# Optimization experiments

Hardware: AMD Instinct MI355X
Metric: run time of the kernel (lower is better)

The kernel has to match this reference:

```python
import jax, jax.numpy as jnp
import numpy as np

L = 4096   # num_tokens (one prefill sequence)
D = 2048   # hidden_size
HK = 16    # num_k_heads
HV = 32    # num_v_heads
DK = 128   # head_k_dim
DV = 128   # head_v_dim
RATIO = HV // HK
EPS = 1e-6


def setup_inputs() -> dict:
    key = jax.random.key(0)
    ks = jax.random.split(key, 11)
    s = 0.02
    return {
        "hidden_states": jax.random.normal(ks[0], (L, D), jnp.float32),
        "Wq": jax.random.normal(ks[1], (D, HK * DK), jnp.float32) * s,
        "Wk": jax.random.normal(ks[2], (D, HK * DK), jnp.float32) * s,
        "Wv": jax.random.normal(ks[3], (D, HV * DV), jnp.float32) * s,
        "Wz": jax.random.normal(ks[4], (D, HV * DV), jnp.float32) * s,
        "Wb": jax.random.normal(ks[5], (D, HV), jnp.float32) * s,
        "Wa": jax.random.normal(ks[6], (D, HV), jnp.float32) * s,
        "A_log": jnp.log(jax.random.uniform(ks[7], (HV,), jnp.float32, 1.0, 16.0)),
        "dt_bias": jax.random.normal(ks[8], (HV,), jnp.float32) * 0.5,
        "norm_weight": jnp.ones((DV,), jnp.float32),
        "W_out": jax.random.normal(ks[9], (HV * DV, D), jnp.float32) * s,
    }


def _l2norm(x):
    return x * jax.lax.rsqrt(jnp.sum(x * x, axis=-1, keepdims=True) + EPS)


def reference(hidden_states, Wq, Wk, Wv, Wz, Wb, Wa, A_log, dt_bias, norm_weight, W_out):
    h = hidden_states
    # --- input projections (qkvz + ba split) ---
    q = _l2norm((h @ Wq).reshape(L, HK, DK))            # [L, HK, DK]
    k = _l2norm((h @ Wk).reshape(L, HK, DK))
    v = (h @ Wv).reshape(L, HV, DV)                     # [L, HV, DV]
    z = (h @ Wz).reshape(L, HV, DV)                     # gate for RMSNorm
    beta = jax.nn.sigmoid(h @ Wb)                       # [L, HV]
    g = -jnp.exp(A_log) * jax.nn.softplus(h @ Wa + dt_bias)  # [L, HV]
    decay = jnp.exp(g)                                  # per-token per-head decay
    # repeat shared q/k heads to value heads (GQA ratio)
    q = jnp.repeat(q, RATIO, axis=1) * (DK ** -0.5)     # [L, HV, DK]
    k = jnp.repeat(k, RATIO, axis=1)

    # --- gated delta rule recurrence over tokens ---
    def step(S, xs):
        q_t, k_t, v_t, b_t, d_t = xs                    # [HV,DK],[HV,DK],[HV,DV],[HV],[HV]
        S = S * d_t[:, None, None]                      # decay state [HV, DK, DV]
        pred = jnp.einsum('hk,hkv->hv', k_t, S)         # memory readout
        delta = (v_t - pred) * b_t[:, None]             # delta-rule correction
        S = S + k_t[:, :, None] * delta[:, None, :]
        o = jnp.einsum('hk,hkv->hv', q_t, S)
        return S, o

    S0 = jnp.zeros((HV, DK, DV), jnp.float32)
    _, core = jax.lax.scan(step, S0, (q, k, v, beta, decay))  # core: [L, HV, DV]

    # --- gated RMSNorm: x * silu(z), rms-normalize over head dim ---
    x = core * jax.nn.silu(z)
    x = x * jax.lax.rsqrt(jnp.mean(x * x, axis=-1, keepdims=True) + EPS) * norm_weight

    # --- output projection ---
    return x.reshape(L, HV * DV) @ W_out                # [L, D]
```

## Files before the change

kernel.cpp:

```cpp
#include <hip/hip_runtime.h>

#define LTOK 4096
#define DHID 2048
#define HKN  16
#define HVN  32
#define DKK  128
#define NTOT 12288

typedef unsigned short u16;
typedef __attribute__((ext_vector_type(8))) short short8;
typedef __attribute__((ext_vector_type(8))) unsigned short u16x8;
typedef __attribute__((ext_vector_type(4))) unsigned short u16x4;
typedef __attribute__((ext_vector_type(4))) float f32x4;

__device__ __forceinline__ float b2f(u16 u) {
  unsigned int x = ((unsigned int)u) << 16;
  return __builtin_bit_cast(float, x);
}
__device__ __forceinline__ u16 f2bf(float f) {
  unsigned int u = __builtin_bit_cast(unsigned int, f);
  u += 0x7FFFu + ((u >> 16) & 1u);
  return (u16)(u >> 16);
}

template<int C> __device__ __forceinline__ float dppmv(float x) {
  int i = __builtin_amdgcn_update_dpp(0, __builtin_bit_cast(int, x), C, 0xF, 0xF, true);
  return __builtin_bit_cast(float, i);
}
__device__ __forceinline__ float red16(float x) {
  x += dppmv<0xB1>(x);
  x += dppmv<0x4E>(x);
  x += dppmv<0x124>(x);
  x += dppmv<0x128>(x);
  return x;
}

__device__ __forceinline__ void gld16(const void* g, void* l) {
  __builtin_amdgcn_global_load_lds((const __attribute__((address_space(1))) void*)g,
                                   (__attribute__((address_space(3))) void*)l, 16, 0, 0);
}

template<int OFF> __device__ __forceinline__ short8 dsr(unsigned a) {
  short8 r;
  asm volatile("ds_read_b128 %0, %1 offset:%2" : "=v"(r) : "v"(a), "n"(OFF));
  return r;
}
__device__ __forceinline__ short8 gldx4(const u16* p) {
  short8 r;
  asm volatile("global_load_dwordx4 %0, %1, off" : "=v"(r) : "v"(p));
  return r;
}
#define KEEPV(x) asm volatile("" :: "v"(x))

__device__ __forceinline__ int sw16(int r, int c, int rowc) { return (r * rowc + c) ^ ((r & 7) << 3); }

__device__ __forceinline__ void cstore(u16* C, size_t i, float v) { C[i] = f2bf(v); }
__device__ __forceinline__ void cstore(float* C, size_t i, float v) { C[i] = v; }

__global__ __launch_bounds__(256)
void k_cvt(const float* __restrict__ s, u16* __restrict__ d, int n) {
  const int i = (blockIdx.x * 256 + threadIdx.x) * 4;
  const float4 v = *(const float4*)(s + i);
  ushort4 o;
  o.x = f2bf(v.x); o.y = f2bf(v.y); o.z = f2bf(v.z); o.w = f2bf(v.w);
  *(ushort4*)(d + i) = o;
}

__global__ __launch_bounds__(256)
void k_trf(const float* __restrict__ W, u16* __restrict__ Bf, int Ncols, int nkt, int j16base) {
  const int wv = threadIdx.x >> 6, lane = threadIdx.x & 63;
  const int frag = blockIdx.x * 4 + wv;
  const int j16 = frag / nkt, kt = frag % nkt;
  const int r0 = kt * 32 + (lane >> 4) * 8;
  const int c = j16 * 16 + (lane & 15);
  u16x8 o;
#pragma unroll
  for (int e = 0; e < 8; ++e) o[e] = f2bf(W[(size_t)(r0 + e) * Ncols + c]);
  *(u16x8*)(Bf + ((size_t)(j16base + j16) * nkt + kt) * 512 + lane * 8) = o;
}

#define MFMA16(a, b, c) __builtin_amdgcn_mfma_f32_16x16x32_bf16(a, b, c, 0, 0, 0)

template<typename OutT, int NWM, int NWN>
__global__ __launch_bounds__(NWM * 256, 2)
void k_g256(const u16* __restrict__ A, const u16* __restrict__ Bf, OutT* __restrict__ C,
            int M, int N, int K, int NT) {
  constexpr int BN = NWN * 64;
  constexpr int BUFE = NWM * 4096;
  __shared__ u16 Lds[4 * BUFE];
  const int tid = threadIdx.x;
  const int lane = tid & 63, w = tid >> 6;
  const int fr = lane & 15, fq = lane >> 4;
  const int wm = (w >> 2) * 128, wn = (w & 3) * (NWN * 16);
  const int nkt = K >> 5;
  const size_t sK = (size_t)K;

  const int MT = gridDim.x / NT;
  const int nts = (NT < 16) ? NT : 16;
  const int per_super = MT * nts;
  const int super = blockIdx.x / per_super;
  const int within = blockIdx.x % per_super;
  const int mtg = MT >> 3;
  const int q = within >> 3;
  const int mt = (within & 7) * mtg + (q % mtg);
  const int nt = super * nts + q / mtg;

  const int kslot = ((tid & 3) ^ ((tid >> 3) & 3)) * 8;
  const u16* aS = A + (size_t)(mt * (NWM * 128) + (tid >> 2)) * sK + kslot;

  const int jw = nt * (BN / 16) + (w & 3) * NWN;
  const u16* bp[NWN];
#pragma unroll
  for (int j = 0; j < NWN; ++j) bp[j] = Bf + ((size_t)(jw + j) * nkt) * 512 + lane * 8;

  f32x4 acc[8][NWN] = {};

  auto STAGE = [&](int kt_) {
    const int sk = (kt_ < nkt) ? kt_ : nkt - 1;
    u16* base = &Lds[(kt_ & 3) * BUFE];
    gld16(aS + (size_t)sk * 32, base + tid * 8);
    gld16(aS + (size_t)(NWM * 64) * sK + (size_t)sk * 32, base + NWM * 2048 + tid * 8);
  };

#define LOADB(bset, kt_) {                                                    \
    const int sk2 = ((kt_) < nkt) ? (kt_) : (nkt - 1);                        \
    _Pragma("unroll")                                                         \
    for (int j = 0; j < NWN; ++j) bset[j] = gldx4(bp[j] + (size_t)sk2 * 512); }

  const int akey = (fr >> 1) & 3;
  const unsigned ldsBase = (unsigned)(size_t)(__attribute__((address_space(3))) void*)&Lds[0];
  const unsigned aA0 = ldsBase + 2u * (unsigned)((wm + fr) * 32 + ((fq ^ akey) << 3));

  short8 afA[8], afB[8], bs0[NWN], bs1[NWN];

#define RD(afX, kt_) {                                                        \
    const unsigned aAr = aA0 + (unsigned)(((kt_) & 3) * (BUFE * 2));          \
    afX[0] = dsr<0>(aAr);    afX[1] = dsr<1024>(aAr);                         \
    afX[2] = dsr<2048>(aAr); afX[3] = dsr<3072>(aAr);                         \
    afX[4] = dsr<4096>(aAr); afX[5] = dsr<5120>(aAr);                         \
    afX[6] = dsr<6144>(aAr); afX[7] = dsr<7168>(aAr); }

  STAGE(0); STAGE(1); STAGE(2);
  LOADB(bs0, 0)
  LOADB(bs1, 1)
  asm volatile("s_waitcnt vmcnt(0)" ::: "memory");
  __builtin_amdgcn_s_barrier();
  RD(afA, 0)
  asm volatile("s_waitcnt lgkmcnt(0)" ::: "memory");
  __builtin_amdgcn_sched_barrier(0);

#define ITER(kt_, afC, bC, afN) {                                             \
    STAGE((kt_) + 3);                                                         \
    asm volatile("s_waitcnt vmcnt(%0)" :: "n"(NWN + 4) : "memory");           \
    __builtin_amdgcn_s_barrier();                                             \
    __builtin_amdgcn_sched_barrier(0);                                        \
    RD(afN, (kt_) + 1)                                                        \
    __builtin_amdgcn_sched_barrier(0);                                        \
    __builtin_amdgcn_s_setprio(1);                                            \
    _Pragma("unroll")                                                         \
    for (int i = 0; i < 8; ++i)                                               \
      _Pragma("unroll")                                                       \
      for (int j = 0; j < NWN; ++j)                                           \
        acc[i][j] = MFMA16(afC[i], bC[j], acc[i][j]);                         \
    __builtin_amdgcn_s_setprio(0);                                            \
    LOADB(bC, (kt_) + 2)                                                      \
    asm volatile("s_waitcnt lgkmcnt(0)" ::: "memory");                        \
    __builtin_amdgcn_sched_barrier(0); }

  for (int kt = 0; kt < nkt; kt += 2) {
    ITER(kt, afA, bs0, afB)
    ITER(kt + 1, afB, bs1, afA)
  }
#undef ITER
#undef RD
#undef LOADB

  asm volatile("s_waitcnt vmcnt(0) lgkmcnt(0)" ::: "memory");
  __builtin_amdgcn_sched_barrier(0);
  KEEPV(bs0[0]); KEEPV(bs0[1]);
  if constexpr (NWN == 4) { KEEPV(bs0[2]); KEEPV(bs0[3]); }
  KEEPV(bs1[0]); KEEPV(bs1[1]);
  if constexpr (NWN == 4) { KEEPV(bs1[2]); KEEPV(bs1[3]); }
  KEEPV(afA[0]); KEEPV(afA[1]); KEEPV(afA[2]); KEEPV(afA[3]);
  KEEPV(afA[4]); KEEPV(afA[5]); KEEPV(afA[6]); KEEPV(afA[7]);
  KEEPV(afB[0]); KEEPV(afB[1]); KEEPV(afB[2]); KEEPV(afB[3]);
  KEEPV(afB[4]); KEEPV(afB[5]); KEEPV(afB[6]); KEEPV(afB[7]);

  const int r0 = mt * (NWM * 128) + wm + fq * 4;
  const int c0 = nt * BN + wn + fr;
#pragma unroll
  for (int i = 0; i < 8; ++i)
#pragma unroll
    for (int j = 0; j < NWN; ++j)
#pragma unroll
      for (int e = 0; e < 4; ++e)
        cstore(C, (size_t)(r0 + i * 16 + e) * N + c0 + j * 16, acc[i][j][e]);
}

__global__ __launch_bounds__(256)
void k_ba(const float* __restrict__ h, const float* __restrict__ Wb, const float* __restrict__ Wa,
          const float* __restrict__ A_log, const float* __restrict__ dtb,
          float* __restrict__ beta, float* __restrict__ g_out) {
  const int w = threadIdx.x >> 6, lane = threadIdx.x & 63;
  const int t = blockIdx.x * 4 + w;
  const int j = lane & 31;
  const bool isB = lane < 32;
  const float* __restrict__ hr = h + (size_t)t * DHID;
  const float* Wc = isB ? Wb : Wa;
  float acc = 0.f;
  for (int kk = 0; kk < DHID; ++kk) acc = fmaf(hr[kk], Wc[(size_t)kk * HVN + j], acc);
  if (isB) {
    beta[(size_t)t * HVN + j] = 1.f / (1.f + expf(-acc));
  } else {
    float xx = acc + dtb[j];
    float sp = (xx > 20.f) ? xx : log1pf(expf(xx));
    g_out[(size_t)t * HVN + j] = -expf(A_log[j]) * sp;
  }
}

__global__ __launch_bounds__(256)
void k_l2n(u16* __restrict__ qkvz) {
  const int w = threadIdx.x >> 6, lane = threadIdx.x & 63;
  const int r = blockIdx.x * 4 + w;
  const int isK = r >> 16;
  const int rr = r & 65535;
  const int t = rr >> 4, hd = rr & 15;
  u16* p = qkvz + (size_t)t * NTOT + isK * 2048 + hd * DKK + lane * 2;
  float a = b2f(p[0]), b = b2f(p[1]);
  float ss = a * a + b * b;
  ss = red16(ss);
  ss += __shfl_xor(ss, 16);
  ss += __shfl_xor(ss, 32);
  const float sc = rsqrtf(ss + 1e-6f) * (isK ? 1.f : 0.08838834764831845f);
  p[0] = f2bf(a * sc); p[1] = f2bf(b * sc);
}

__global__ __launch_bounds__(256)
void k_r1(const u16* __restrict__ qkvz, const float* __restrict__ beta_g,
          const float* __restrict__ g_g, u16* __restrict__ UM_g, float* __restrict__ cumL_g) {
  const int pair = blockIdx.x;
  const int hv = pair >> 6, n = pair & 63;
  const int hk = hv >> 1;
  const int t0 = n * 64;
  const int tid = threadIdx.x, lane = tid & 63, wv = tid >> 6;
  const int fr = lane & 15, fq = lane >> 4;

  __shared__ __align__(16) u16 Xb[256 * 64];
  __shared__ __align__(16) u16 Dbuf0[64 * 64 * 2];
  __shared__ __align__(16) u16 Dbuf1[64 * 64 * 2];
  __shared__ float Lc[64];
  __shared__ float Bc[64];
  u16* Kl = Dbuf0;

  const int j = tid & 63, h = tid >> 6;
  const u16* kg = qkvz + (size_t)(t0 + j) * NTOT + 2048 + hk * DKK + h * 32;
  const u16* vg = qkvz + (size_t)(t0 + j) * NTOT + 4096 + hv * DKK + h * 32;
  u16x8 kv[4], vv[4];
#pragma unroll
  for (int i = 0; i < 4; ++i) { kv[i] = *(const u16x8*)(kg + i * 8); vv[i] = *(const u16x8*)(vg + i * 8); }
  if (tid < 64) {
    Lc[tid] = g_g[(size_t)(t0 + tid) * HVN + hv];
    Bc[tid] = beta_g[(size_t)(t0 + tid) * HVN + hv];
  }
#pragma unroll
  for (int i = 0; i < 4; ++i) *(u16x8*)&Kl[sw16(j, h * 32 + i * 8, 128)] = kv[i];
  __syncthreads();
  if (tid == 0) { float a = 0.f; for (int t = 0; t < 64; ++t) { a += Lc[t]; Lc[t] = a; } }
  __syncthreads();
  if (tid < 64) cumL_g[(size_t)pair * 64 + tid] = Lc[tid];

  {
    const float bj = Bc[j];
    const float mj = bj * __expf(Lc[j]);
#pragma unroll
    for (int i = 0; i < 4; ++i)
#pragma unroll
      for (int e = 0; e < 8; ++e) {
        int c = h * 32 + i * 8 + e;
        Xb[sw16(c, j, 64)] = f2bf(bj * b2f(vv[i][e]));
        Xb[sw16(128 + c, j, 64)] = f2bf(mj * b2f(kv[i][e]));
      }
  }
  f32x4 kk[4] = {};
#pragma unroll
  for (int ks = 0; ks < 4; ++ks) {
    short8 afr = *(const short8*)&Kl[sw16(wv * 16 + fr, ks * 32 + fq * 8, 128)];
#pragma unroll
    for (int ct = 0; ct < 4; ++ct) {
      short8 bfr = *(const short8*)&Kl[sw16(ct * 16 + fr, ks * 32 + fq * 8, 128)];
      kk[ct] = MFMA16(afr, bfr, kk[ct]);
    }
  }
  __syncthreads();

  f32x4 acc[16];
#pragma unroll
  for (int ct = 0; ct < 16; ++ct) {
    u16x4 xi = *(const u16x4*)&Xb[sw16(ct * 16 + fr, wv * 16 + fq * 4, 64)];
    acc[ct][0] = b2f(xi[0]); acc[ct][1] = b2f(xi[1]); acc[ct][2] = b2f(xi[2]); acc[ct][3] = b2f(xi[3]);
  }
#pragma unroll
  for (int ct = 0; ct < 4; ++ct) {
    const int s = ct * 16 + fr;
    u16x4 pk;
#pragma unroll
    for (int e = 0; e < 4; ++e) {
      const int t = wv * 16 + fq * 4 + e;
      float v = (s < t) ? -Bc[t] * __expf(Lc[t] - Lc[s]) * kk[ct][e] : 0.f;
      pk[e] = f2bf(v);
      Dbuf0[sw16(t, s, 64)] = pk[e];
    }
    *(u16x4*)&Dbuf0[4096 + sw16(s, wv * 16 + fq * 4, 64)] = pk;
  }
  __syncthreads();

  u16* DA = Dbuf0;
  u16* DB = Dbuf1;
  for (int stg = 0; stg < 6; ++stg) {
    u16* Dr = DA;
    u16* Dc = DA + 4096;
    short8 da0 = *(const short8*)&Dr[sw16(wv * 16 + fr, 0 + fq * 8, 64)];
    short8 da1 = *(const short8*)&Dr[sw16(wv * 16 + fr, 32 + fq * 8, 64)];
#pragma unroll
    for (int ct = 0; ct < 16; ++ct) {
      short8 b0 = *(const short8*)&Xb[sw16(ct * 16 + fr, 0 + fq * 8, 64)];
      short8 b1 = *(const short8*)&Xb[sw16(ct * 16 + fr, 32 + fq * 8, 64)];
      acc[ct] = MFMA16(da0, b0, acc[ct]);
      acc[ct] = MFMA16(da1, b1, acc[ct]);
    }
    f32x4 sq[4] = {};
    if (stg < 5) {
#pragma unroll
      for (int ct = 0; ct < 4; ++ct) {
        short8 sb0 = *(const short8*)&Dc[sw16(ct * 16 + fr, 0 + fq * 8, 64)];
        short8 sb1 = *(const short8*)&Dc[sw16(ct * 16 + fr, 32 + fq * 8, 64)];
        sq[ct] = MFMA16(da0, sb0, sq[ct]);
        sq[ct] = MFMA16(da1, sb1, sq[ct]);
      }
    }
    __syncthreads();
#pragma unroll
    for (int ct = 0; ct < 16; ++ct) {
      u16x4 pk;
      pk[0] = f2bf(acc[ct][0]); pk[1] = f2bf(acc[ct][1]); pk[2] = f2bf(acc[ct][2]); pk[3] = f2bf(acc[ct][3]);
      *(u16x4*)&Xb[sw16(ct * 16 + fr, wv * 16 + fq * 4, 64)] = pk;
    }
    if (stg < 5) {
#pragma unroll
      for (int ct = 0; ct < 4; ++ct) {
        u16x4 pk;
        pk[0] = f2bf(sq[ct][0]); pk[1] = f2bf(sq[ct][1]); pk[2] = f2bf(sq[ct][2]); pk[3] = f2bf(sq[ct][3]);
        *(u16x4*)&(DB + 4096)[sw16(ct * 16 + fr, wv * 16 + fq * 4, 64)] = pk;
#pragma unroll
        for (int e = 0; e < 4; ++e) DB[sw16(wv * 16 + fq * 4 + e, ct * 16 + fr, 64)] = pk[e];
      }
    }
    __syncthreads();
    u16* tmp = DA; DA = DB; DB = tmp;
  }

#pragma unroll
  for (int ct = 0; ct < 16; ++ct) {
    const int c = ct * 16 + fr;
#pragma unroll
    for (int e = 0; e < 4; ++e) {
      const int t = wv * 16 + fq * 4 + e;
      float v = acc[ct][e];
      if (ct >= 8) v = -v;
      UM_g[((size_t)pair * 64 + t) * 256 + c] = f2bf(v);
    }
  }
}

__global__ __launch_bounds__(512)
void k_r2(u16* __restrict__ qkvz, const u16* __restrict__ UM_g,
          const float* __restrict__ cumL_g, u16* __restrict__ o1_g) {
  const int hv = blockIdx.x >> 2, cs = blockIdx.x & 3;
  const int hk = hv >> 1;
  const int tid = threadIdx.x, lane = tid & 63, w = tid >> 6;
  const int fr = lane & 15, fq = lane >> 4;
  const int tw = w & 3, dwv = w >> 2;

  __shared__ __align__(16) u16 dT[2048];
  __shared__ __align__(16) u16 dT2[2048];
  __shared__ __align__(16) u16 o1b[2048];
  __shared__ __align__(16) u16 SbT[4096];

  f32x4 sacc[2];
#pragma unroll
  for (int d = 0; d < 2; ++d) sacc[d] = (f32x4){0.f, 0.f, 0.f, 0.f};
  for (int i = tid; i < 4096; i += 512) SbT[i] = 0;

  u16x8 QA[4], MA[4], QB[4], MB[4], KA0, KA1, KB0, KB1;
  u16 UA[4], UB[4];
  float LA4[4], LB4[4], LA63, LB63;

#define PREF(nn, Q, Mv, K0, K1, U, L4, L63v) {                                \
    const int nc = ((nn) < 64) ? (nn) : 63;                                   \
    const int pr = hv * 64 + nc; const int tt0 = nc * 64;                     \
    const u16* qg = qkvz + (size_t)(tt0 + tw * 16 + fr) * NTOT + hk * DKK + fq * 8; \
    Q[0] = *(const u16x8*)qg;        Q[1] = *(const u16x8*)(qg + 32);         \
    Q[2] = *(const u16x8*)(qg + 64); Q[3] = *(const u16x8*)(qg + 96);         \
    const u16* mg = UM_g + ((size_t)pr * 64 + tw * 16 + fr) * 256 + 128 + fq * 8; \
    Mv[0] = *(const u16x8*)mg;        Mv[1] = *(const u16x8*)(mg + 32);       \
    Mv[2] = *(const u16x8*)(mg + 64); Mv[3] = *(const u16x8*)(mg + 96);       \
    const u16* ug = UM_g + ((size_t)pr * 64 + tw * 16 + fq * 4) * 256         \
                    + cs * 32 + dwv * 16 + fr;                                \
    U[0] = ug[0]; U[1] = ug[256]; U[2] = ug[512]; U[3] = ug[768];             \
    const u16* kg = qkvz + (size_t)(tt0 + fq * 8) * NTOT + 2048 + hk * DKK + w * 16 + fr; \
    _Pragma("unroll")                                                         \
    for (int e = 0; e < 8; ++e) {                                             \
      K0[e] = kg[(size_t)e * NTOT];                                           \
      K1[e] = kg[(size_t)(32 + e) * NTOT];                                    \
    }                                                                         \
    _Pragma("unroll")                                                         \
    for (int e = 0; e < 4; ++e) L4[e] = cumL_g[(size_t)pr * 64 + tw * 16 + fq * 4 + e]; \
    L63v = cumL_g[(size_t)pr * 64 + 63]; }

#define PH1(Q, Mv, U, L4, L63v) {                                             \
    float el[4], el2[4];                                                      \
    _Pragma("unroll")                                                         \
    for (int e = 0; e < 4; ++e) {                                             \
      el[e] = __expf(L4[e]);                                                  \
      el2[e] = __expf(L63v - L4[e]);                                          \
    }                                                                         \
    f32x4 dc;                                                                 \
    dc[0] = b2f(U[0]); dc[1] = b2f(U[1]); dc[2] = b2f(U[2]); dc[3] = b2f(U[3]); \
    f32x4 oc = {};                                                            \
    _Pragma("unroll")                                                         \
    for (int ks = 0; ks < 4; ++ks) {                                          \
      short8 bs = *(const short8*)&SbT[sw16(dwv * 16 + fr, ks * 32 + fq * 8, 128)]; \
      dc = MFMA16(__builtin_bit_cast(short8, Mv[ks]), bs, dc);                \
      oc = MFMA16(__builtin_bit_cast(short8, Q[ks]), bs, oc);                 \
    }                                                                         \
    u16x4 pkd, pkd2, pko;                                                     \
    _Pragma("unroll")                                                         \
    for (int e = 0; e < 4; ++e) {                                             \
      pkd[e]  = f2bf(dc[e]);                                                  \
      pkd2[e] = f2bf(dc[e] * el2[e]);                                         \
      pko[e]  = f2bf(oc[e] * el[e]);                                          \
    }                                                                         \
    *(u16x4*)&dT[sw16(dwv * 16 + fr, tw * 16 + fq * 4, 64)] = pkd;            \
    *(u16x4*)&dT2[sw16(dwv * 16 + fr, tw * 16 + fq * 4, 64)] = pkd2;          \
    *(u16x4*)&o1b[sw16(dwv * 16 + fr, tw * 16 + fq * 4, 64)] = pko; }

#define PH2(K0, K1, L63v, t0_, pair_) {                                       \
    {                                                                         \
      const int i = tid * 4;                                                  \
      u16x4 vd = *(const u16x4*)&dT[i];                                       \
      const int f = cs * 2048 + i;                                            \
      *(u16x4*)(qkvz + (size_t)((t0_) + (f >> 7)) * NTOT + 4096 + hv * DKK + (f & 127)) = vd; \
      u16x4 vo = *(const u16x4*)&o1b[i];                                      \
      *(u16x4*)(o1_g + (size_t)(pair_) * 8192 + cs * 2048 + i) = vo;          \
    }                                                                         \
    const float eC = __expf(L63v);                                            \
    short8 ak0 = __builtin_bit_cast(short8, K0);                              \
    short8 ak1 = __builtin_bit_cast(short8, K1);                              \
    _Pragma("unroll")                                                         \
    for (int d = 0; d < 2; ++d) {                                             \
      short8 bd0 = *(const short8*)&dT2[sw16(d * 16 + fr, fq * 8, 64)];       \
      short8 bd1 = *(const short8*)&dT2[sw16(d * 16 + fr, 32 + fq * 8, 64)];  \
      f32x4 sa = sacc[d];                                                     \
      _Pragma("unroll")                                                       \
      for (int e = 0; e < 4; ++e) sa[e] *= eC;                                \
      sa = MFMA16(ak0, bd0, sa);                                              \
      sa = MFMA16(ak1, bd1, sa);                                              \
      sacc[d] = sa;                                                           \
      u16x4 pk;                                                               \
      pk[0] = f2bf(sa[0]); pk[1] = f2bf(sa[1]); pk[2] = f2bf(sa[2]); pk[3] = f2bf(sa[3]); \
      *(u16x4*)&SbT[sw16(d * 16 + fr, w * 16 + fq * 4, 128)] = pk;            \
    }                                                                         \
  }

  PREF(0, QA, MA, KA0, KA1, UA, LA4, LA63)
  __syncthreads();

  for (int n = 0; n < 64; n += 2) {
    {
      PREF(n + 1, QB, MB, KB0, KB1, UB, LB4, LB63)
      PH1(QA, MA, UA, LA4, LA63)
      __syncthreads();
      const int t0 = n * 64, pair = hv * 64 + n;
      PH2(KA0, KA1, LA63, t0, pair)
      __syncthreads();
    }
    {
      PREF(n + 2, QA, MA, KA0, KA1, UA, LA4, LA63)
      PH1(QB, MB, UB, LB4, LB63)
      __syncthreads();
      const int t0 = (n + 1) * 64, pair = hv * 64 + n + 1;
      PH2(KB0, KB1, LB63, t0, pair)
      __syncthreads();
    }
  }
#undef PREF
#undef PH1
#undef PH2
}

__global__ __launch_bounds__(512)
void k_r3(const u16* __restrict__ qkvz, const u16* __restrict__ o1_g,
          const float* __restrict__ cumL_g, const float* __restrict__ nw,
          u16* __restrict__ x) {
  const int pair = blockIdx.x, hv = pair >> 6, n = pair & 63, hk = hv >> 1, t0 = n * 64;
  const int tid = threadIdx.x, lane = tid & 63, w = tid >> 6;
  const int fr = lane & 15, fq = lane >> 4;
  const int j = tid & 63, h = tid >> 6;

  __shared__ __align__(16) u16 Ql[8192];
  __shared__ __align__(16) u16 Kl[8192];
  __shared__ __align__(16) u16 Gl[4096];
  __shared__ __align__(16) u16 dTl[8192];
  __shared__ __align__(16) u16 o1l[8192];
  __shared__ __align__(16) float of[64 * 132];
  __shared__ float Lc[64];
  __shared__ float Lw[128];

  {
    const u16* qg = qkvz + (size_t)(t0 + j) * NTOT + hk * DKK + h * 16;
    u16x8 q0 = *(const u16x8*)qg, q1 = *(const u16x8*)(qg + 8);
    u16x8 k0 = *(const u16x8*)(qg + 2048), k1 = *(const u16x8*)(qg + 2056);
    *(u16x8*)&Ql[sw16(j, h * 16, 128)] = q0;
    *(u16x8*)&Ql[sw16(j, h * 16 + 8, 128)] = q1;
    *(u16x8*)&Kl[sw16(j, h * 16, 128)] = k0;
    *(u16x8*)&Kl[sw16(j, h * 16 + 8, 128)] = k1;
  }
#pragma unroll
  for (int it = 0; it < 2; ++it) {
    const int f = ((w * 2 + it) * 64 + lane) * 8;
    gld16(qkvz + (size_t)(t0 + (f >> 7)) * NTOT + 4096 + hv * DKK + (f & 127),
          (char*)dTl + (w * 2 + it) * 1024);
    gld16(o1_g + (size_t)pair * 8192 + f, (char*)o1l + (w * 2 + it) * 1024);
  }
  if (tid < 64) Lc[tid] = cumL_g[(size_t)pair * 64 + tid];
  if (tid < 128) Lw[tid] = nw[tid];
  __syncthreads();

  const int tw = w & 3, sp = (w >> 2) * 2;
  {
    f32x4 kk0 = {}, kk1 = {};
#pragma unroll
    for (int ks = 0; ks < 4; ++ks) {
      short8 aq = *(const short8*)&Ql[sw16(tw * 16 + fr, ks * 32 + fq * 8, 128)];
      short8 b0 = *(const short8*)&Kl[sw16(sp * 16 + fr, ks * 32 + fq * 8, 128)];
      short8 b1 = *(const short8*)&Kl[sw16((sp + 1) * 16 + fr, ks * 32 + fq * 8, 128)];
      kk0 = MFMA16(aq, b0, kk0);
      kk1 = MFMA16(aq, b1, kk1);
    }
#pragma unroll
    for (int e = 0; e < 4; ++e) {
      const int t = tw * 16 + fq * 4 + e;
      const float Lt = Lc[t];
      const int s0 = sp * 16 + fr, s1 = s0 + 16;
      Gl[sw16(t, s0, 64)] = f2bf((s0 <= t) ? kk0[e] * __expf(Lt - Lc[s0]) : 0.f);
      Gl[sw16(t, s1, 64)] = f2bf((s1 <= t) ? kk1[e] * __expf(Lt - Lc[s1]) : 0.f);
    }
  }
  __syncthreads();

  {
    short8 ag0 = *(const short8*)&Gl[sw16(tw * 16 + fr, fq * 8, 64)];
    short8 ag1 = *(const short8*)&Gl[sw16(tw * 16 + fr, 32 + fq * 8, 64)];
#pragma unroll
    for (int dd = 0; dd < 4; ++dd) {
      const int d = (w >> 2) * 4 + dd;
      short8 bd0 = *(const short8*)&dTl[sw16(d * 16 + fr, fq * 8, 64)];
      short8 bd1 = *(const short8*)&dTl[sw16(d * 16 + fr, 32 + fq * 8, 64)];
      f32x4 oc = {};
      oc = MFMA16(ag0, bd0, oc);
      oc = MFMA16(ag1, bd1, oc);
#pragma unroll
      for (int e = 0; e < 4; ++e) of[(tw * 16 + fq * 4 + e) * 132 + d * 16 + fr] = oc[e];
    }
  }
  __syncthreads();

  {
    const int t = tid >> 3, q8 = tid & 7;
    const u16* zp = qkvz + (size_t)(t0 + t) * NTOT + 8192 + hv * DKK + q8 * 16;
    float xv[16];
    float ss = 0.f;
#pragma unroll
    for (int i = 0; i < 2; ++i) {
      u16x8 zv = *(const u16x8*)(zp + i * 8);
#pragma unroll
      for (int e = 0; e < 8; ++e) {
        const int dv = q8 * 16 + i * 8 + e;
        float z = b2f(zv[e]);
        float o = of[t * 132 + dv] + b2f(o1l[sw16(dv, t, 64)]);
        float xx = o * (z / (1.f + __expf(-z)));
        xv[i * 8 + e] = xx;
        ss = fmaf(xx, xx, ss);
      }
    }
    ss += __shfl_xor(ss, 1);
    ss += __shfl_xor(ss, 2);
    ss += __shfl_xor(ss, 4);
    const float scl = rsqrtf(ss * (1.f / 128.f) + 1e-6f);
    u16* xo = x + (size_t)(t0 + t) * 4096 + hv * DKK + q8 * 16;
#pragma unroll
    for (int i = 0; i < 2; ++i) {
      u16x8 pk;
#pragma unroll
      for (int e = 0; e < 8; ++e) pk[e] = f2bf(xv[i * 8 + e] * scl * Lw[q8 * 16 + i * 8 + e]);
      *(u16x8*)(xo + i * 8) = pk;
    }
  }
}

extern "C" void kernel_launch(void* const* d_in, const int* in_sizes, int n_in,
                              void* d_out, int out_size, void* d_ws, size_t ws_size,
                              hipStream_t stream) {
  const float* h    = (const float*)d_in[0];
  const float* Wq   = (const float*)d_in[1];
  const float* Wk   = (const float*)d_in[2];
  const float* Wv   = (const float*)d_in[3];
  const float* Wz   = (const float*)d_in[4];
  const float* Wb   = (const float*)d_in[5];
  const float* Wa   = (const float*)d_in[6];
  const float* Alog = (const float*)d_in[7];
  const float* dtb  = (const float*)d_in[8];
  const float* nw   = (const float*)d_in[9];
  const float* Wo   = (const float*)d_in[10];
  char* ws = (char*)d_ws;
  u16* h_bf  = (u16*)(ws);
  u16* Bfq   = (u16*)(ws + 16777216ull);
  u16* UM    = (u16*)(ws);
  u16* Bfo   = (u16*)(ws + 67108864ull);
  u16* qkvz  = (u16*)(ws + 83886080ull);
  u16* o1g   = (u16*)(ws + 184549376ull);
  u16* xbuf  = (u16*)(ws + 16777216ull);
  float* beta  = (float*)(ws + 218103808ull);
  float* g     = (float*)(ws + 218103808ull + 524288ull);
  float* cumL  = (float*)(ws + 218103808ull + 1048576ull);

  k_cvt<<<8192, 256, 0, stream>>>(h, h_bf, LTOK * DHID);
  k_trf<<<2048, 256, 0, stream>>>(Wq, Bfq, 2048, 64, 0);
  k_trf<<<2048, 256, 0, stream>>>(Wk, Bfq, 2048, 64, 128);
  k_trf<<<4096, 256, 0, stream>>>(Wv, Bfq, 4096, 64, 256);
  k_trf<<<4096, 256, 0, stream>>>(Wz, Bfq, 4096, 64, 512);
  k_trf<<<4096, 256, 0, stream>>>(Wo, Bfo, 2048, 128, 0);
  k_g256<u16, 2, 4><<<768, 512, 0, stream>>>(h_bf, Bfq, qkvz, 4096, 12288, 2048, 48);
  k_ba<<<1024, 256, 0, stream>>>(h, Wb, Wa, Alog, dtb, beta, g);
  k_l2n<<<32768, 256, 0, stream>>>(qkvz);
  k_r1<<<2048, 256, 0, stream>>>(qkvz, beta, g, UM, cumL);
  k_r2<<<128, 512, 0, stream>>>(qkvz, UM, cumL, o1g);
  k_r3<<<2048, 512, 0, stream>>>(qkvz, o1g, cumL, nw, xbuf);
  k_g256<float, 1, 2><<<512, 256, 0, stream>>>(xbuf, Bfo, (float*)d_out, 4096, 2048, 4096, 16);
}
```

Before: 792.8 us.

## Split chunk-recurrence kernel across more blocks by halving value-column slice per block

The sequential inter-chunk state kernel now covers 16 value columns per block instead of 32, launching 256 blocks of 256 threads instead of 128 blocks of 512. This aims to use more of the GPU's compute units for the serial recurrence over 64 chunks, since 128 blocks leave many CUs idle. In exchange each block redundantly loads the full Q, M and K tiles for half as much output work, so global read traffic for those operands doubles. Each wave also now holds two K fragments to compute 32 rows of the state.

```diff
diff --git a/kernel.cpp b/kernel.cpp
--- a/kernel.cpp
+++ b/kernel.cpp
@@ -372,30 +372,31 @@
   }
 }
 
-__global__ __launch_bounds__(512)
+__global__ __launch_bounds__(256)
 void k_r2(u16* __restrict__ qkvz, const u16* __restrict__ UM_g,
           const float* __restrict__ cumL_g, u16* __restrict__ o1_g) {
-  const int hv = blockIdx.x >> 2, cs = blockIdx.x & 3;
+  const int hv = blockIdx.x >> 3, cs = blockIdx.x & 7;
   const int hk = hv >> 1;
   const int tid = threadIdx.x, lane = tid & 63, w = tid >> 6;
   const int fr = lane & 15, fq = lane >> 4;
-  const int tw = w & 3, dwv = w >> 2;
-
-  __shared__ __align__(16) u16 dT[2048];
-  __shared__ __align__(16) u16 dT2[2048];
-  __shared__ __align__(16) u16 o1b[2048];
-  __shared__ __align__(16) u16 SbT[4096];
+  const int tw = w;
+
+  __shared__ __align__(16) u16 dT[1024];
+  __shared__ __align__(16) u16 dT2[1024];
+  __shared__ __align__(16) u16 o1b[1024];
+  __shared__ __align__(16) u16 SbT[2048];
 
   f32x4 sacc[2];
 #pragma unroll
   for (int d = 0; d < 2; ++d) sacc[d] = (f32x4){0.f, 0.f, 0.f, 0.f};
-  for (int i = tid; i < 4096; i += 512) SbT[i] = 0;
-
-  u16x8 QA[4], MA[4], QB[4], MB[4], KA0, KA1, KB0, KB1;
+  for (int i = tid; i < 2048; i += 256) SbT[i] = 0;
+
+  u16x8 QA[4], MA[4], QB[4], MB[4];
+  u16x8 KA00, KA01, KA10, KA11, KB00, KB01, KB10, KB11;
   u16 UA[4], UB[4];
   float LA4[4], LB4[4], LA63, LB63;
 
-#define PREF(nn, Q, Mv, K0, K1, U, L4, L63v) {                                \
+#define PREF(nn, Q, Mv, K00, K01, K10, K11, U, L4, L63v) {                    \
     const int nc = ((nn) < 64) ? (nn) : 63;                                   \
     const int pr = hv * 64 + nc; const int tt0 = nc * 64;                     \
     const u16* qg = qkvz + (size_t)(tt0 + tw * 16 + fr) * NTOT + hk * DKK + fq * 8; \
@@ -405,13 +406,15 @@
     Mv[0] = *(const u16x8*)mg;        Mv[1] = *(const u16x8*)(mg + 32);       \
     Mv[2] = *(const u16x8*)(mg + 64); Mv[3] = *(const u16x8*)(mg + 96);       \
     const u16* ug = UM_g + ((size_t)pr * 64 + tw * 16 + fq * 4) * 256         \
-                    + cs * 32 + dwv * 16 + fr;                                \
+                    + cs * 16 + fr;                                           \
     U[0] = ug[0]; U[1] = ug[256]; U[2] = ug[512]; U[3] = ug[768];             \
-    const u16* kg = qkvz + (size_t)(tt0 + fq * 8) * NTOT + 2048 + hk * DKK + w * 16 + fr; \
+    const u16* kg = qkvz + (size_t)(tt0 + fq * 8) * NTOT + 2048 + hk * DKK + w * 32 + fr; \
     _Pragma("unroll")                                                         \
     for (int e = 0; e < 8; ++e) {                                             \
-      K0[e] = kg[(size_t)e * NTOT];                                           \
-      K1[e] = kg[(size_t)(32 + e) * NTOT];                                    \
+      K00[e] = kg[(size_t)e * NTOT];                                          \
+      K01[e] = kg[(size_t)(32 + e) * NTOT];                                   \
+      K10[e] = kg[(size_t)e * NTOT + 16];                                     \
+      K11[e] = kg[(size_t)(32 + e) * NTOT + 16];                              \
     }                                                                         \
     _Pragma("unroll")                                                         \
     for (int e = 0; e < 4; ++e) L4[e] = cumL_g[(size_t)pr * 64 + tw * 16 + fq * 4 + e]; \
@@ -429,7 +432,7 @@
     f32x4 oc = {};                                                            \
     _Pragma("unroll")                                                         \
     for (int ks = 0; ks < 4; ++ks) {                                          \
-      short8 bs = *(const short8*)&SbT[sw16(dwv * 16 + fr, ks * 32 + fq * 8, 128)]; \
+      short8 bs = *(const short8*)&SbT[sw16(fr, ks * 32 + fq * 8, 128)];      \
       dc = MFMA16(__builtin_bit_cast(short8, Mv[ks]), bs, dc);                \
       oc = MFMA16(__builtin_bit_cast(short8, Q[ks]), bs, oc);                 \
     }                                                                         \
@@ -440,56 +443,64 @@
       pkd2[e] = f2bf(dc[e] * el2[e]);                                         \
       pko[e]  = f2bf(oc[e] * el[e]);                                          \
     }                                                                         \
-    *(u16x4*)&dT[sw16(dwv * 16 + fr, tw * 16 + fq * 4, 64)] = pkd;            \
-    *(u16x4*)&dT2[sw16(dwv * 16 + fr, tw * 16 + fq * 4, 64)] = pkd2;          \
-    *(u16x4*)&o1b[sw16(dwv * 16 + fr, tw * 16 + fq * 4, 64)] = pko; }
-
-#define PH2(K0, K1, L63v, t0_, pair_) {                                       \
+    *(u16x4*)&dT[sw16(fr, tw * 16 + fq * 4, 64)] = pkd;                       \
+    *(u16x4*)&dT2[sw16(fr, tw * 16 + fq * 4, 64)] = pkd2;                     \
+    *(u16x4*)&o1b[sw16(fr, tw * 16 + fq * 4, 64)] = pko; }
+
+#define PH2(K00, K01, K10, K11, L63v, t0_, pair_) {                           \
     {                                                                         \
       const int i = tid * 4;                                                  \
       u16x4 vd = *(const u16x4*)&dT[i];                                       \
-      const int f = cs * 2048 + i;                                            \
+      const int f = cs * 1024 + i;                                            \
       *(u16x4*)(qkvz + (size_t)((t0_) + (f >> 7)) * NTOT + 4096 + hv * DKK + (f & 127)) = vd; \
       u16x4 vo = *(const u16x4*)&o1b[i];                                      \
-      *(u16x4*)(o1_g + (size_t)(pair_) * 8192 + cs * 2048 + i) = vo;          \
+      *(u16x4*)(o1_g + (size_t)(pair_) * 8192 + f) = vo;                      \
     }                                                                         \
     const float eC = __expf(L63v);                                            \
-    short8 ak0 = __builtin_bit_cast(short8, K0);                              \
-    short8 ak1 = __builtin_bit_cast(short8, K1);                              \
-    _Pragma("unroll")                                                         \
-    for (int d = 0; d < 2; ++d) {                                             \
-      short8 bd0 = *(const short8*)&dT2[sw16(d * 16 + fr, fq * 8, 64)];       \
-      short8 bd1 = *(const short8*)&dT2[sw16(d * 16 + fr, 32 + fq * 8, 64)];  \
-      f32x4 sa = sacc[d];                                                     \
+    short8 bd0 = *(const short8*)&dT2[sw16(fr, fq * 8, 64)];                  \
+    short8 bd1 = *(const short8*)&dT2[sw16(fr, 32 + fq * 8, 64)];             \
+    {                                                                         \
+      f32x4 sa = sacc[0];                                                     \
       _Pragma("unroll")                                                       \
       for (int e = 0; e < 4; ++e) sa[e] *= eC;                                \
-      sa = MFMA16(ak0, bd0, sa);                                              \
-      sa = MFMA16(ak1, bd1, sa);                                              \
-      sacc[d] = sa;                                                           \
+      sa = MFMA16(__builtin_bit_cast(short8, K00), bd0, sa);                  \
+      sa = MFMA16(__builtin_bit_cast(short8, K01), bd1, sa);                  \
+      sacc[0] = sa;                                                           \
       u16x4 pk;                                                               \
       pk[0] = f2bf(sa[0]); pk[1] = f2bf(sa[1]); pk[2] = f2bf(sa[2]); pk[3] = f2bf(sa[3]); \
-      *(u16x4*)&SbT[sw16(d * 16 + fr, w * 16 + fq * 4, 128)] = pk;            \
+      *(u16x4*)&SbT[sw16(fr, w * 32 + fq * 4, 128)] = pk;                     \
     }                                                                         \
-  }
-
-  PREF(0, QA, MA, KA0, KA1, UA, LA4, LA63)
+    {                                                                         \
+      f32x4 sa = sacc[1];                                                     \
+      _Pragma("unroll")                                                       \
+      for (int e = 0; e < 4; ++e) sa[e] *= eC;                                \
+      sa = MFMA16(__builtin_bit_cast(short8, K10), bd0, sa);                  \
+      sa = MFMA16(__builtin_bit_cast(short8, K11), bd1, sa);                  \
+      sacc[1] = sa;                                                           \
+      u16x4 pk;                                                               \
+      pk[0] = f2bf(sa[0]); pk[1] = f2bf(sa[1]); pk[2] = f2bf(sa[2]); pk[3] = f2bf(sa[3]); \
+      *(u16x4*)&SbT[sw16(fr, w * 32 + 16 + fq * 4, 128)] = pk;                \
+    }                                                                         \
+  }
+
+  PREF(0, QA, MA, KA00, KA01, KA10, KA11, UA, LA4, LA63)
   __syncthreads();
 
   for (int n = 0; n < 64; n += 2) {
     {
-      PREF(n + 1, QB, MB, KB0, KB1, UB, LB4, LB63)
+      PREF(n + 1, QB, MB, KB00, KB01, KB10, KB11, UB, LB4, LB63)
       PH1(QA, MA, UA, LA4, LA63)
       __syncthreads();
       const int t0 = n * 64, pair = hv * 64 + n;
-      PH2(KA0, KA1, LA63, t0, pair)
+      PH2(KA00, KA01, KA10, KA11, LA63, t0, pair)
       __syncthreads();
     }
     {
-      PREF(n + 2, QA, MA, KA0, KA1, UA, LA4, LA63)
+      PREF(n + 2, QA, MA, KA00, KA01, KA10, KA11, UA, LA4, LA63)
       PH1(QB, MB, UB, LB4, LB63)
       __syncthreads();
       const int t0 = (n + 1) * 64, pair = hv * 64 + n + 1;
-      PH2(KB0, KB1, LB63, t0, pair)
+      PH2(KB00, KB01, KB10, KB11, LB63, t0, pair)
       __syncthreads();
     }
   }
@@ -644,7 +655,7 @@
   k_ba<<<1024, 256, 0, stream>>>(h, Wb, Wa, Alog, dtb, beta, g);
   k_l2n<<<32768, 256, 0, stream>>>(qkvz);
   k_r1<<<2048, 256, 0, stream>>>(qkvz, beta, g, UM, cumL);
-  k_r2<<<128, 512, 0, stream>>>(qkvz, UM, cumL, o1g);
+  k_r2<<<256, 256, 0, stream>>>(qkvz, UM, cumL, o1g);
   k_r3<<<2048, 512, 0, stream>>>(qkvz, o1g, cumL, nw, xbuf);
   k_g256<float, 1, 2><<<512, 256, 0, stream>>>(xbuf, Bfo, (float*)d_out, 4096, 2048, 4096, 16);
 }
```

After: 759.0 us. 4.3% less time.
